# Performance work log

Hardware: AMD Instinct MI355X
Metric: run time of the kernel (lower is better)

The kernel has to match this reference:

```python
import math
import jax, jax.numpy as jnp
import numpy as np
from jax import lax

B, T, C = 2, 4096, 2048
N_HEAD, N_KV, D = 16, 4, 128
WINDOW, DILATION, CHUNK = 256, 1, 128


def make_rope_cache(seq_len, n_elem, base=10000.0):
    theta = 1.0 / base ** (jnp.arange(0, n_elem, 2, dtype=jnp.float32) / n_elem)
    idx_theta = jnp.arange(seq_len, dtype=jnp.float32)[:, None] * theta[None, :]
    return jnp.stack([jnp.cos(idx_theta), jnp.sin(idx_theta)], axis=-1)  # [T, n_elem/2, 2]


def setup_inputs() -> dict:
    key = jax.random.key(0)
    ks = jax.random.split(key, 5)
    s = 1.0 / math.sqrt(C)
    return {
        "x": jax.random.normal(ks[0], (B, T, C), dtype=jnp.float32),
        "wq": jax.random.normal(ks[1], (N_HEAD * D, C), dtype=jnp.float32) * s,
        "wk": jax.random.normal(ks[2], (N_KV * D, C), dtype=jnp.float32) * s,
        "wv": jax.random.normal(ks[3], (N_KV * D, C), dtype=jnp.float32) * s,
        "wo": jax.random.normal(ks[4], (N_HEAD * D, C), dtype=jnp.float32).T * s,  # stored [out,in]
        "rope_cache": make_rope_cache(T, D),
    }


def apply_rope(xh, cache):
    # xh: [B, T, H, D]; cache: [T, D/2, 2]
    b, t, h, d = xh.shape
    xr = xh.reshape(b, t, h, d // 2, 2)
    cos = cache[:t, :, 0][None, :, None, :]
    sin = cache[:t, :, 1][None, :, None, :]
    x0, x1 = xr[..., 0], xr[..., 1]
    rot = jnp.stack([x0 * cos - x1 * sin, x0 * sin + x1 * cos], axis=-1)
    return rot.reshape(b, t, h, d)


def sliding_attention(q, k, v, window, dilation, chunk):
    # q,k,v: [B, H, T, D] -> [B, H, T, D]; O(T*window), memory bounded via scan over chunks
    b, h, t, d = q.shape
    w = min(window, (t + dilation - 1) // dilation)
    offsets = jnp.arange(w) * dilation
    scale = 1.0 / math.sqrt(d)
    n_chunks = t // chunk

    def step(carry, c):
        pos = c * chunk + jnp.arange(chunk)                       # [L]
        idx_raw = (pos - (w - 1) * dilation)[:, None] + offsets[None, :]  # [L, w]
        invalid = idx_raw < 0
        idx = jnp.clip(idx_raw, 0, t - 1)
        flat = idx.reshape(-1)
        k_win = jnp.take(k, flat, axis=2).reshape(b, h, chunk, w, d)
        v_win = jnp.take(v, flat, axis=2).reshape(b, h, chunk, w, d)
        q_c = lax.dynamic_slice_in_dim(q, c * chunk, chunk, axis=2)
        scores = jnp.einsum('bhld,bhlwd->bhlw', q_c.astype(jnp.float32),
                            k_win.astype(jnp.float32)) * scale
        scores = jnp.where(invalid[None, None], -jnp.inf, scores)
        attn = jax.nn.softmax(scores, axis=-1)
        out_c = jnp.einsum('bhlw,bhlwd->bhld', attn, v_win.astype(jnp.float32))
        return carry, out_c.astype(q.dtype)

    _, outs = lax.scan(step, None, jnp.arange(n_chunks))  # [n_chunks, B, H, chunk, D]
    return outs.transpose(1, 2, 0, 3, 4).reshape(b, h, t, d)


def reference(x, wq, wk, wv, wo, rope_cache):
    b, t, c = x.shape
    q = (x @ wq.T).reshape(b, t, N_HEAD, D)
    k = (x @ wk.T).reshape(b, t, N_KV, D)
    v = (x @ wv.T).reshape(b, t, N_KV, D)
    q = apply_rope(q, rope_cache)
    k = apply_rope(k, rope_cache)
    q = q.transpose(0, 2, 1, 3)  # [B, H, T, D]
    k = k.transpose(0, 2, 1, 3)
    v = v.transpose(0, 2, 1, 3)
    g = N_HEAD // N_KV
    k = jnp.repeat(k, g, axis=1)
    v = jnp.repeat(v, g, axis=1)
    y = sliding_attention(q, k, v, WINDOW, DILATION, CHUNK)
    y = y.transpose(0, 2, 1, 3).reshape(b, t, c)
    return y @ wo.T
```

## Files before the change

### kernel.cpp

```cpp
#include <hip/hip_runtime.h>
#include <stdint.h>

typedef unsigned short u16;
typedef __attribute__((ext_vector_type(8))) short bf16x8;
typedef __attribute__((ext_vector_type(8))) unsigned short u16x8;
typedef __attribute__((ext_vector_type(4))) float f32x4;

#define B_  2
#define T_  4096
#define C_  2048
#define NH  16
#define NKV 4
#define HD  128

__device__ __forceinline__ u16 f2bf(float f) {
  union { float f; uint32_t u; } v; v.f = f;
  uint32_t u = v.u;
  u += 0x7fffu + ((u >> 16) & 1u);
  return (u16)(u >> 16);
}
__device__ __forceinline__ float bf2f(u16 h) {
  union { uint32_t u; float f; } v; v.u = ((uint32_t)h) << 16;
  return v.f;
}

__device__ __forceinline__ void gload_lds16(const u16* g, u16* l) {
  __builtin_amdgcn_global_load_lds(
      (const __attribute__((address_space(1))) void*)g,
      (__attribute__((address_space(3))) void*)l, 16, 0, 0);
}

__global__ void cvt_f32_bf16(const float* __restrict__ src, u16* __restrict__ dst, int n) {
  int i = (blockIdx.x * blockDim.x + threadIdx.x) * 4;
  if (i >= n) return;
  float4 v = *(const float4*)(src + i);
  ushort4 o;
  o.x = f2bf(v.x); o.y = f2bf(v.y); o.z = f2bf(v.z); o.w = f2bf(v.w);
  *(ushort4*)(dst + i) = o;
}

__global__ void rope_kernel(u16* __restrict__ qkv, const float* __restrict__ cache) {
  const int PH = (NH + NKV) * (HD / 2);
  long idx = (long)blockIdx.x * blockDim.x + threadIdx.x;
  if (idx >= (long)B_ * T_ * PH) return;
  int row = (int)(idx / PH);
  int rem = (int)(idx % PH);
  int hh = rem >> 6;
  int i  = rem & 63;
  int t  = row & (T_ - 1);
  float sc = (hh < NH) ? 0.1275174315f : 1.0f;
  float c = cache[t * 128 + 2 * i] * sc;
  float s = cache[t * 128 + 2 * i + 1] * sc;
  u16* p = qkv + (long)row * 3072 + hh * HD + 2 * i;
  float x0 = bf2f(p[0]), x1 = bf2f(p[1]);
  p[0] = f2bf(x0 * c - x1 * s);
  p[1] = f2bf(x0 * s + x1 * c);
}

__global__ void krearr(const u16* __restrict__ qkv, u16* __restrict__ K2) {
  int gid = blockIdx.x * 256 + threadIdx.x;
  int r = gid & 65535, bk = gid >> 16;
  int l16 = r & 15, q4 = (r >> 4) & 3, ks = (r >> 6) & 3, kb = r >> 8;
  int bb = bk >> 2, kv = bk & 3;
  const u16* src = qkv + ((long)(bb * T_ + kb * 16 + l16)) * 3072 + 2048 + kv * HD +
                   ks * 32 + q4 * 8;
  *(u16x8*)(K2 + (long)bk * 524288 + (long)r * 8) = *(const u16x8*)src;
}

__global__ void vrearr(const u16* __restrict__ qkv, u16* __restrict__ V2) {
  int gid = blockIdx.x * 256 + threadIdx.x;
  int r = gid & 65535, bk = gid >> 16;
  int l16 = r & 15, q4 = (r >> 4) & 3, ks = (r >> 6) & 3, jd = (r >> 8) & 7, kc = r >> 11;
  int bb = bk >> 2, kv = bk & 3;
  int key0 = kc * 128 + ks * 32 + q4 * 8;
  int d = jd * 16 + l16;
  const u16* src = qkv + ((long)(bb * T_ + key0)) * 3072 + 2560 + kv * HD + d;
  u16x8 v;
#pragma unroll
  for (int e = 0; e < 8; e++) v[e] = src[(long)e * 3072];
  *(u16x8*)(V2 + (long)bk * 524288 + (long)r * 8) = v;
}

#define GBAR() __builtin_amdgcn_s_barrier()
#define LGKM0() do { asm volatile("s_waitcnt lgkmcnt(0)" ::: "memory"); \
                     __builtin_amdgcn_sched_barrier(0); } while (0)

template <int WRITE_BF16>
__global__ __launch_bounds__(512, 2) void gemm256(const u16* __restrict__ A,
                                                  const u16* __restrict__ Bw,
                                                  void* __restrict__ Cv,
                                                  int M, int N, int K) {
  __shared__ u16 lds[65536];
  const int tid = threadIdx.x;
  const int lane = tid & 63;
  const int wave = tid >> 6;
  const int q4 = lane >> 4, l16 = lane & 15;
  const int wm = wave >> 2, wn = wave & 3;

  const int nwg = gridDim.x * gridDim.y;
  const int orig = blockIdx.y * gridDim.x + blockIdx.x;
  const int swz = (orig & 7) * (nwg >> 3) + (orig >> 3);
  const int bm = swz / gridDim.x, bn = swz % gridDim.x;
  const long m0 = (long)bm * 256, n0 = (long)bn * 256;

  const int srow = tid >> 2;
  const int slot = tid & 3;
  const int sx = (slot ^ ((srow >> 1) & 3)) * 8;
  const u16* Ag0 = A + (m0 + srow) * K + sx;
  const u16* Ag1 = A + (m0 + srow + 128) * K + sx;
  const u16* Bg0 = Bw + (n0 + srow) * K + sx;
  const u16* Bg1 = Bw + (n0 + srow + 128) * K + sx;
  u16* ldst = lds + tid * 8;

  const int nkt = K >> 6;

#define STAGE_A(bufi, kh, kt)                                  \
  do {                                                         \
    long ko = ((long)(kt) << 6) + ((kh) << 5);                 \
    u16* d = ldst + (bufi) * 32768 + (kh) * 8192;              \
    gload_lds16(Ag0 + ko, d);                                  \
    gload_lds16(Ag1 + ko, d + 4096);                           \
  } while (0)
#define STAGE_B(bufi, kh, kt)                                  \
  do {                                                         \
    long ko = ((long)(kt) << 6) + ((kh) << 5);                 \
    u16* d = ldst + (bufi) * 32768 + 16384 + (kh) * 8192;      \
    gload_lds16(Bg0 + ko, d);                                  \
    gload_lds16(Bg1 + ko, d + 4096);                           \
  } while (0)

  int offA[8], offB[4];
#pragma unroll
  for (int m = 0; m < 8; m++) {
    int r = wm * 128 + m * 16 + l16;
    offA[m] = r * 32 + ((q4 ^ ((r >> 1) & 3)) << 3);
  }
#pragma unroll
  for (int n = 0; n < 4; n++) {
    int r = wn * 64 + n * 16 + l16;
    offB[n] = 16384 + r * 32 + ((q4 ^ ((r >> 1) & 3)) << 3);
  }

  f32x4 acc[8][4] = {};

  STAGE_A(0, 0, 0); STAGE_B(0, 0, 0); STAGE_A(0, 1, 0); STAGE_B(0, 1, 0);
  if (nkt > 1) {
    STAGE_A(1, 0, 1); STAGE_B(1, 0, 1);
    asm volatile("s_waitcnt vmcnt(4)" ::: "memory");
  } else {
    asm volatile("s_waitcnt vmcnt(0)" ::: "memory");
  }
  GBAR();

  bf16x8 afX[4], afY[4], bvA[4], bvB[4];
  for (int kt = 0; kt < nkt; kt++) {
    const int bo = (kt & 1) * 32768;
#pragma unroll
    for (int m = 0; m < 4; m++) afX[m] = *(const bf16x8*)(lds + bo + offA[m]);
#pragma unroll
    for (int n = 0; n < 4; n++) bvA[n] = *(const bf16x8*)(lds + bo + offB[n]);
    if (kt + 1 < nkt) STAGE_A((kt + 1) & 1, 1, kt + 1);
    LGKM0();
#pragma unroll
    for (int m = 0; m < 4; m++) afY[m] = *(const bf16x8*)(lds + bo + offA[4 + m]);
    __builtin_amdgcn_s_setprio(1);
#pragma unroll
    for (int m = 0; m < 4; m++)
#pragma unroll
      for (int n = 0; n < 4; n++)
        acc[m][n] = __builtin_amdgcn_mfma_f32_16x16x32_bf16(afX[m], bvA[n], acc[m][n], 0, 0, 0);
    __builtin_amdgcn_s_setprio(0);
    if (kt + 1 < nkt) STAGE_B((kt + 1) & 1, 1, kt + 1);
    LGKM0();
#pragma unroll
    for (int m = 0; m < 4; m++) afX[m] = *(const bf16x8*)(lds + bo + 8192 + offA[m]);
#pragma unroll
    for (int n = 0; n < 4; n++) bvB[n] = *(const bf16x8*)(lds + bo + 8192 + offB[n]);
    __builtin_amdgcn_s_setprio(1);
#pragma unroll
    for (int m = 0; m < 4; m++)
#pragma unroll
      for (int n = 0; n < 4; n++)
        acc[4 + m][n] = __builtin_amdgcn_mfma_f32_16x16x32_bf16(afY[m], bvA[n], acc[4 + m][n], 0, 0, 0);
    __builtin_amdgcn_s_setprio(0);
    GBAR();
    if (kt + 2 < nkt) STAGE_A(kt & 1, 0, kt + 2);
    LGKM0();
#pragma unroll
    for (int m = 0; m < 4; m++) afY[m] = *(const bf16x8*)(lds + bo + 8192 + offA[4 + m]);
    __builtin_amdgcn_s_setprio(1);
#pragma unroll
    for (int m = 0; m < 4; m++)
#pragma unroll
      for (int n = 0; n < 4; n++)
        acc[m][n] = __builtin_amdgcn_mfma_f32_16x16x32_bf16(afX[m], bvB[n], acc[m][n], 0, 0, 0);
    __builtin_amdgcn_s_setprio(0);
    if (kt + 2 < nkt) STAGE_B(kt & 1, 0, kt + 2);
    LGKM0();
    __builtin_amdgcn_s_setprio(1);
#pragma unroll
    for (int m = 0; m < 4; m++)
#pragma unroll
      for (int n = 0; n < 4; n++)
        acc[4 + m][n] = __builtin_amdgcn_mfma_f32_16x16x32_bf16(afY[m], bvB[n], acc[4 + m][n], 0, 0, 0);
    __builtin_amdgcn_s_setprio(0);
    if (kt + 2 < nkt)
      asm volatile("s_waitcnt vmcnt(4)" ::: "memory");
    else
      asm volatile("s_waitcnt vmcnt(0)" ::: "memory");
    GBAR();
  }
#undef STAGE_A
#undef STAGE_B

  const long crow0 = m0 + wm * 128;
  const long ccol0 = n0 + wn * 64;
  if (WRITE_BF16) {
    u16* Cp = (u16*)Cv;
#pragma unroll
    for (int m = 0; m < 8; m++)
#pragma unroll
      for (int n = 0; n < 4; n++)
#pragma unroll
        for (int r = 0; r < 4; r++)
          Cp[(crow0 + m * 16 + q4 * 4 + r) * (long)N + ccol0 + n * 16 + l16] =
              f2bf(acc[m][n][r]);
  } else {
    float* Cp = (float*)Cv;
#pragma unroll
    for (int m = 0; m < 8; m++)
#pragma unroll
      for (int n = 0; n < 4; n++)
#pragma unroll
        for (int r = 0; r < 4; r++)
          Cp[(crow0 + m * 16 + q4 * 4 + r) * (long)N + ccol0 + n * 16 + l16] =
              acc[m][n][r];
  }
}

__global__ __launch_bounds__(256, 3) void attn_kernel(const u16* __restrict__ qkv,
                                                      const u16* __restrict__ K2,
                                                      const u16* __restrict__ V2,
                                                      u16* __restrict__ y) {
  const int tc = blockIdx.x, h = blockIdx.y, b = blockIdx.z;
  const int t0 = tc * 128;
  const int kvh = h >> 2;
  __shared__ u16 Pl[4 * 32 * 136];
  const int tid = threadIdx.x, wave = tid >> 6, lane = tid & 63;
  const int q4 = lane >> 4, l16 = lane & 15;
  u16* Pw = Pl + wave * (32 * 136);

  bf16x8 qf[2][4];
#pragma unroll
  for (int i = 0; i < 2; i++)
#pragma unroll
    for (int ks = 0; ks < 4; ks++)
      qf[i][ks] = *(const bf16x8*)(qkv +
          ((long)(b * T_ + t0 + 32 * wave + 16 * i + l16)) * 3072 + h * HD + ks * 32 + q4 * 8);

  f32x4 O[2][8] = {};
  float l_i[2][4] = {};

  const u16* Kb = K2 + (long)(b * NKV + kvh) * 524288 + lane * 8;
  const u16* Vb = V2 + (long)(b * NKV + kvh) * 524288 + lane * 8;

  int kstart = t0 - 256; if (kstart < 0) kstart = 0;
  for (int k0 = kstart; k0 <= t0; k0 += 128) {
    const u16* Kc = Kb + (long)(k0 >> 4) * 2048;
    const u16* Vc = Vb + (long)(k0 >> 7) * 16384;
    const int dbase0 = t0 + 32 * wave + q4 * 4 - k0 - l16;
    bf16x8 kn[4];
#pragma unroll
    for (int ks = 0; ks < 4; ks++) kn[ks] = *(const bf16x8*)(Kc + ks * 512);
#pragma unroll
    for (int j = 0; j < 8; j++) {
      bf16x8 kf[4];
#pragma unroll
      for (int ks = 0; ks < 4; ks++) kf[ks] = kn[ks];
      if (j < 7)
#pragma unroll
        for (int ks = 0; ks < 4; ks++)
          kn[ks] = *(const bf16x8*)(Kc + (j + 1) * 2048 + ks * 512);
      f32x4 s0 = {}, s1 = {};
#pragma unroll
      for (int ks = 0; ks < 4; ks++) {
        s0 = __builtin_amdgcn_mfma_f32_16x16x32_bf16(qf[0][ks], kf[ks], s0, 0, 0, 0);
        s1 = __builtin_amdgcn_mfma_f32_16x16x32_bf16(qf[1][ks], kf[ks], s1, 0, 0, 0);
      }
#pragma unroll
      for (int r = 0; r < 4; r++) {
        int d0 = dbase0 + r - 16 * j;
        float p0 = __builtin_amdgcn_exp2f(s0[r]);
        p0 = ((unsigned)d0 <= 255u) ? p0 : 0.f;
        l_i[0][r] += p0;
        Pw[(q4 * 4 + r) * 136 + 16 * j + l16] = f2bf(p0);
        int d1 = d0 + 16;
        float p1 = __builtin_amdgcn_exp2f(s1[r]);
        p1 = ((unsigned)d1 <= 255u) ? p1 : 0.f;
        l_i[1][r] += p1;
        Pw[(16 + q4 * 4 + r) * 136 + 16 * j + l16] = f2bf(p1);
      }
    }
    bf16x8 vn = *(const bf16x8*)(Vc);
#pragma unroll
    for (int ks = 0; ks < 4; ks++) {
      bf16x8 pf0 = *(const bf16x8*)(&Pw[l16 * 136 + ks * 32 + q4 * 8]);
      bf16x8 pf1 = *(const bf16x8*)(&Pw[(16 + l16) * 136 + ks * 32 + q4 * 8]);
#pragma unroll
      for (int jd = 0; jd < 8; jd++) {
        bf16x8 vf = vn;
        if (!(ks == 3 && jd == 7)) {
          int njd = (jd == 7) ? 0 : jd + 1;
          int nks = (jd == 7) ? ks + 1 : ks;
          vn = *(const bf16x8*)(Vc + (njd * 4 + nks) * 512);
        }
        O[0][jd] = __builtin_amdgcn_mfma_f32_16x16x32_bf16(pf0, vf, O[0][jd], 0, 0, 0);
        O[1][jd] = __builtin_amdgcn_mfma_f32_16x16x32_bf16(pf1, vf, O[1][jd], 0, 0, 0);
      }
    }
  }
#pragma unroll
  for (int d = 1; d < 16; d <<= 1)
#pragma unroll
    for (int i = 0; i < 2; i++)
#pragma unroll
      for (int r = 0; r < 4; r++)
        l_i[i][r] += __shfl_xor(l_i[i][r], d, 64);
#pragma unroll
  for (int i = 0; i < 2; i++)
#pragma unroll
    for (int r = 0; r < 4; r++) {
      float inv = 1.0f / l_i[i][r];
      long row = (long)(b * T_ + t0 + 32 * wave + 16 * i + q4 * 4 + r);
#pragma unroll
      for (int jd = 0; jd < 8; jd++)
        y[row * 2048 + h * HD + 16 * jd + l16] = f2bf(O[i][jd][r] * inv);
    }
}

extern "C" void kernel_launch(void* const* d_in, const int* in_sizes, int n_in,
                              void* d_out, int out_size, void* d_ws, size_t ws_size,
                              hipStream_t stream) {
  const float* x    = (const float*)d_in[0];
  const float* wq   = (const float*)d_in[1];
  const float* wk   = (const float*)d_in[2];
  const float* wv   = (const float*)d_in[3];
  const float* wo   = (const float*)d_in[4];
  const float* rope = (const float*)d_in[5];
  float* out = (float*)d_out;

  u16* xb   = (u16*)d_ws;
  u16* wqkv = xb + (long)8192 * 2048;
  u16* wob  = wqkv + (long)3072 * 2048;
  u16* qkv  = wob + (long)2048 * 2048;
  u16* V2   = qkv + (long)8192 * 3072;
  u16* K2   = wqkv;
  u16* yb   = xb;

  {
    long n = (long)8192 * 2048;
    cvt_f32_bf16<<<dim3((unsigned)((n / 4 + 255) / 256)), dim3(256), 0, stream>>>(x, xb, (int)n);
    n = (long)2048 * 2048;
    cvt_f32_bf16<<<dim3((unsigned)((n / 4 + 255) / 256)), dim3(256), 0, stream>>>(wq, wqkv, (int)n);
    n = (long)512 * 2048;
    cvt_f32_bf16<<<dim3((unsigned)((n / 4 + 255) / 256)), dim3(256), 0, stream>>>(
        wk, wqkv + (long)2048 * 2048, (int)n);
    cvt_f32_bf16<<<dim3((unsigned)((n / 4 + 255) / 256)), dim3(256), 0, stream>>>(
        wv, wqkv + (long)2048 * 2048 + (long)512 * 2048, (int)n);
    n = (long)2048 * 2048;
    cvt_f32_bf16<<<dim3((unsigned)((n / 4 + 255) / 256)), dim3(256), 0, stream>>>(wo, wob, (int)n);
  }

  gemm256<1><<<dim3(3072 / 256, 8192 / 256), dim3(512), 0, stream>>>(
      xb, wqkv, (void*)qkv, 8192, 3072, 2048);

  long npairs = (long)B_ * T_ * (NH + NKV) * (HD / 2);
  rope_kernel<<<dim3((unsigned)((npairs + 255) / 256)), dim3(256), 0, stream>>>(qkv, rope);

  krearr<<<dim3(2048), dim3(256), 0, stream>>>(qkv, K2);
  vrearr<<<dim3(2048), dim3(256), 0, stream>>>(qkv, V2);

  attn_kernel<<<dim3(T_ / 128, NH, B_), dim3(256), 0, stream>>>(qkv, K2, V2, yb);

  gemm256<0><<<dim3(2048 / 256, 8192 / 256), dim3(512), 0, stream>>>(
      yb, wob, (void*)out, 8192, 2048, 2048);
}
```

Before: 446.7 us.

## Fuse RoPE into QKV GEMM epilogue and switch to 128x256 tiles

Removes the standalone RoPE kernel and applies the rotation and the Q scale in the QKV GEMM epilogue, using lane shuffles to pair adjacent columns. This saves one read-modify-write pass over the Q/K activations. The GEMM is also restructured from 512-thread 256x256 tiles with a two-deep K pipeline to 256-thread 128x256 tiles with a K step of 32 and a full vmcnt(0) wait every iteration. That change reduces latency hiding and per-block reuse in exchange for smaller LDS use and more blocks.

```diff
diff --git a/kernel.cpp b/kernel.cpp
--- a/kernel.cpp
+++ b/kernel.cpp
@@ -37,24 +37,6 @@
   ushort4 o;
   o.x = f2bf(v.x); o.y = f2bf(v.y); o.z = f2bf(v.z); o.w = f2bf(v.w);
   *(ushort4*)(dst + i) = o;
-}
-
-__global__ void rope_kernel(u16* __restrict__ qkv, const float* __restrict__ cache) {
-  const int PH = (NH + NKV) * (HD / 2);
-  long idx = (long)blockIdx.x * blockDim.x + threadIdx.x;
-  if (idx >= (long)B_ * T_ * PH) return;
-  int row = (int)(idx / PH);
-  int rem = (int)(idx % PH);
-  int hh = rem >> 6;
-  int i  = rem & 63;
-  int t  = row & (T_ - 1);
-  float sc = (hh < NH) ? 0.1275174315f : 1.0f;
-  float c = cache[t * 128 + 2 * i] * sc;
-  float s = cache[t * 128 + 2 * i + 1] * sc;
-  u16* p = qkv + (long)row * 3072 + hh * HD + 2 * i;
-  float x0 = bf2f(p[0]), x1 = bf2f(p[1]);
-  p[0] = f2bf(x0 * c - x1 * s);
-  p[1] = f2bf(x0 * s + x1 * c);
 }
 
 __global__ void krearr(const u16* __restrict__ qkv, u16* __restrict__ K2) {
@@ -85,81 +67,86 @@
 #define LGKM0() do { asm volatile("s_waitcnt lgkmcnt(0)" ::: "memory"); \
                      __builtin_amdgcn_sched_barrier(0); } while (0)
 
-template <int WRITE_BF16>
-__global__ __launch_bounds__(512, 2) void gemm256(const u16* __restrict__ A,
+template <int WRITE_BF16, int ROPE>
+__global__ __launch_bounds__(256, 2) void gemm128(const u16* __restrict__ A,
                                                   const u16* __restrict__ Bw,
                                                   void* __restrict__ Cv,
+                                                  const float* __restrict__ rope,
                                                   int M, int N, int K) {
-  __shared__ u16 lds[65536];
+  __shared__ u16 lds[24576];
   const int tid = threadIdx.x;
   const int lane = tid & 63;
   const int wave = tid >> 6;
   const int q4 = lane >> 4, l16 = lane & 15;
-  const int wm = wave >> 2, wn = wave & 3;
 
   const int nwg = gridDim.x * gridDim.y;
   const int orig = blockIdx.y * gridDim.x + blockIdx.x;
   const int swz = (orig & 7) * (nwg >> 3) + (orig >> 3);
   const int bm = swz / gridDim.x, bn = swz % gridDim.x;
-  const long m0 = (long)bm * 256, n0 = (long)bn * 256;
+  const long m0 = (long)bm * 128, n0 = (long)bn * 256;
 
   const int srow = tid >> 2;
   const int slot = tid & 3;
-  const int sx = (slot ^ ((srow >> 1) & 3)) * 8;
-  const u16* Ag0 = A + (m0 + srow) * K + sx;
-  const u16* Ag1 = A + (m0 + srow + 128) * K + sx;
-  const u16* Bg0 = Bw + (n0 + srow) * K + sx;
-  const u16* Bg1 = Bw + (n0 + srow + 128) * K + sx;
+  const int sx = (slot ^ ((srow >> 1) & 3)) << 3;
+  const u16* Ag0 = A + (m0 + srow) * (long)K + sx;
+  const u16* Ag1 = A + (m0 + 64 + srow) * (long)K + sx;
+  const u16* Bg0 = Bw + (n0 + srow) * (long)K + sx;
+  const u16* Bg1 = Bw + (n0 + 64 + srow) * (long)K + sx;
+  const u16* Bg2 = Bw + (n0 + 128 + srow) * (long)K + sx;
+  const u16* Bg3 = Bw + (n0 + 192 + srow) * (long)K + sx;
   u16* ldst = lds + tid * 8;
 
-  const int nkt = K >> 6;
-
-#define STAGE_A(bufi, kh, kt)                                  \
-  do {                                                         \
-    long ko = ((long)(kt) << 6) + ((kh) << 5);                 \
-    u16* d = ldst + (bufi) * 32768 + (kh) * 8192;              \
-    gload_lds16(Ag0 + ko, d);                                  \
-    gload_lds16(Ag1 + ko, d + 4096);                           \
+  const int nkt = K >> 5;
+
+#define STAGE_A(bufi, kt)                                       \
+  do {                                                          \
+    long ko = (long)(kt) << 5;                                  \
+    u16* d = ldst + (bufi) * 12288;                             \
+    gload_lds16(Ag0 + ko, d);                                   \
+    gload_lds16(Ag1 + ko, d + 2048);                            \
   } while (0)
-#define STAGE_B(bufi, kh, kt)                                  \
-  do {                                                         \
-    long ko = ((long)(kt) << 6) + ((kh) << 5);                 \
-    u16* d = ldst + (bufi) * 32768 + 16384 + (kh) * 8192;      \
-    gload_lds16(Bg0 + ko, d);                                  \
-    gload_lds16(Bg1 + ko, d + 4096);                           \
+#define STAGE_B01(bufi, kt)                                     \
+  do {                                                          \
+    long ko = (long)(kt) << 5;                                  \
+    u16* d = ldst + (bufi) * 12288 + 4096;                      \
+    gload_lds16(Bg0 + ko, d);                                   \
+    gload_lds16(Bg1 + ko, d + 2048);                            \
   } while (0)
+#define STAGE_B23(bufi, kt)                                     \
+  do {                                                          \
+    long ko = (long)(kt) << 5;                                  \
+    u16* d = ldst + (bufi) * 12288 + 4096;                      \
+    gload_lds16(Bg2 + ko, d + 4096);                            \
+    gload_lds16(Bg3 + ko, d + 6144);                            \
+  } while (0)
 
   int offA[8], offB[4];
 #pragma unroll
   for (int m = 0; m < 8; m++) {
-    int r = wm * 128 + m * 16 + l16;
+    int r = m * 16 + l16;
     offA[m] = r * 32 + ((q4 ^ ((r >> 1) & 3)) << 3);
   }
 #pragma unroll
   for (int n = 0; n < 4; n++) {
-    int r = wn * 64 + n * 16 + l16;
-    offB[n] = 16384 + r * 32 + ((q4 ^ ((r >> 1) & 3)) << 3);
+    int r = wave * 64 + n * 16 + l16;
+    offB[n] = 4096 + r * 32 + ((q4 ^ ((r >> 1) & 3)) << 3);
   }
 
   f32x4 acc[8][4] = {};
 
-  STAGE_A(0, 0, 0); STAGE_B(0, 0, 0); STAGE_A(0, 1, 0); STAGE_B(0, 1, 0);
-  if (nkt > 1) {
-    STAGE_A(1, 0, 1); STAGE_B(1, 0, 1);
-    asm volatile("s_waitcnt vmcnt(4)" ::: "memory");
-  } else {
-    asm volatile("s_waitcnt vmcnt(0)" ::: "memory");
-  }
+  STAGE_A(0, 0); STAGE_B01(0, 0); STAGE_B23(0, 0);
+  asm volatile("s_waitcnt vmcnt(0)" ::: "memory");
   GBAR();
 
-  bf16x8 afX[4], afY[4], bvA[4], bvB[4];
+  bf16x8 afX[4], afY[4], bv[4];
   for (int kt = 0; kt < nkt; kt++) {
-    const int bo = (kt & 1) * 32768;
+    const int bo = (kt & 1) * 12288;
+    const int nx = (kt & 1) ^ 1;
 #pragma unroll
     for (int m = 0; m < 4; m++) afX[m] = *(const bf16x8*)(lds + bo + offA[m]);
 #pragma unroll
-    for (int n = 0; n < 4; n++) bvA[n] = *(const bf16x8*)(lds + bo + offB[n]);
-    if (kt + 1 < nkt) STAGE_A((kt + 1) & 1, 1, kt + 1);
+    for (int n = 0; n < 4; n++) bv[n] = *(const bf16x8*)(lds + bo + offB[n]);
+    if (kt + 1 < nkt) { STAGE_A(nx, kt + 1); STAGE_B01(nx, kt + 1); }
     LGKM0();
 #pragma unroll
     for (int m = 0; m < 4; m++) afY[m] = *(const bf16x8*)(lds + bo + offA[4 + m]);
@@ -168,74 +155,50 @@
     for (int m = 0; m < 4; m++)
 #pragma unroll
       for (int n = 0; n < 4; n++)
-        acc[m][n] = __builtin_amdgcn_mfma_f32_16x16x32_bf16(afX[m], bvA[n], acc[m][n], 0, 0, 0);
+        acc[m][n] = __builtin_amdgcn_mfma_f32_16x16x32_bf16(afX[m], bv[n], acc[m][n], 0, 0, 0);
     __builtin_amdgcn_s_setprio(0);
-    if (kt + 1 < nkt) STAGE_B((kt + 1) & 1, 1, kt + 1);
-    LGKM0();
-#pragma unroll
-    for (int m = 0; m < 4; m++) afX[m] = *(const bf16x8*)(lds + bo + 8192 + offA[m]);
-#pragma unroll
-    for (int n = 0; n < 4; n++) bvB[n] = *(const bf16x8*)(lds + bo + 8192 + offB[n]);
-    __builtin_amdgcn_s_setprio(1);
-#pragma unroll
-    for (int m = 0; m < 4; m++)
-#pragma unroll
-      for (int n = 0; n < 4; n++)
-        acc[4 + m][n] = __builtin_amdgcn_mfma_f32_16x16x32_bf16(afY[m], bvA[n], acc[4 + m][n], 0, 0, 0);
-    __builtin_amdgcn_s_setprio(0);
-    GBAR();
-    if (kt + 2 < nkt) STAGE_A(kt & 1, 0, kt + 2);
-    LGKM0();
-#pragma unroll
-    for (int m = 0; m < 4; m++) afY[m] = *(const bf16x8*)(lds + bo + 8192 + offA[4 + m]);
-    __builtin_amdgcn_s_setprio(1);
-#pragma unroll
-    for (int m = 0; m < 4; m++)
-#pragma unroll
-      for (int n = 0; n < 4; n++)
-        acc[m][n] = __builtin_amdgcn_mfma_f32_16x16x32_bf16(afX[m], bvB[n], acc[m][n], 0, 0, 0);
-    __builtin_amdgcn_s_setprio(0);
-    if (kt + 2 < nkt) STAGE_B(kt & 1, 0, kt + 2);
+    if (kt + 1 < nkt) STAGE_B23(nx, kt + 1);
     LGKM0();
     __builtin_amdgcn_s_setprio(1);
 #pragma unroll
     for (int m = 0; m < 4; m++)
 #pragma unroll
       for (int n = 0; n < 4; n++)
-        acc[4 + m][n] = __builtin_amdgcn_mfma_f32_16x16x32_bf16(afY[m], bvB[n], acc[4 + m][n], 0, 0, 0);
+        acc[4 + m][n] = __builtin_amdgcn_mfma_f32_16x16x32_bf16(afY[m], bv[n], acc[4 + m][n], 0, 0, 0);
     __builtin_amdgcn_s_setprio(0);
-    if (kt + 2 < nkt)
-      asm volatile("s_waitcnt vmcnt(4)" ::: "memory");
-    else
-      asm volatile("s_waitcnt vmcnt(0)" ::: "memory");
+    asm volatile("s_waitcnt vmcnt(0)" ::: "memory");
     GBAR();
   }
 #undef STAGE_A
-#undef STAGE_B
-
-  const long crow0 = m0 + wm * 128;
-  const long ccol0 = n0 + wn * 64;
-  if (WRITE_BF16) {
-    u16* Cp = (u16*)Cv;
-#pragma unroll
-    for (int m = 0; m < 8; m++)
-#pragma unroll
-      for (int n = 0; n < 4; n++)
-#pragma unroll
-        for (int r = 0; r < 4; r++)
-          Cp[(crow0 + m * 16 + q4 * 4 + r) * (long)N + ccol0 + n * 16 + l16] =
-              f2bf(acc[m][n][r]);
-  } else {
-    float* Cp = (float*)Cv;
-#pragma unroll
-    for (int m = 0; m < 8; m++)
-#pragma unroll
-      for (int n = 0; n < 4; n++)
-#pragma unroll
-        for (int r = 0; r < 4; r++)
-          Cp[(crow0 + m * 16 + q4 * 4 + r) * (long)N + ccol0 + n * 16 + l16] =
-              acc[m][n][r];
-  }
+#undef STAGE_B01
+#undef STAGE_B23
+
+  const long ccol0 = n0 + wave * 64;
+#pragma unroll
+  for (int m = 0; m < 8; m++)
+#pragma unroll
+    for (int n = 0; n < 4; n++) {
+      const int cfrag = (int)(ccol0 + n * 16);
+#pragma unroll
+      for (int r = 0; r < 4; r++) {
+        long row = m0 + m * 16 + q4 * 4 + r;
+        float x = acc[m][n][r];
+        if (ROPE && cfrag < 2560) {
+          int tt = (int)row & (T_ - 1);
+          int c = cfrag + l16;
+          float cv = rope[tt * 128 + (c & 127)];
+          float px = __shfl_xor(x, 1, 64);
+          float pcv = __shfl_xor(cv, 1, 64);
+          float rot = ((l16 & 1) == 0) ? (x * cv - px * pcv) : (px * cv + x * pcv);
+          if (cfrag < 2048) rot *= 0.1275174315f;
+          x = rot;
+        }
+        if (WRITE_BF16)
+          ((u16*)Cv)[row * (long)N + ccol0 + n * 16 + l16] = f2bf(x);
+        else
+          ((float*)Cv)[row * (long)N + ccol0 + n * 16 + l16] = x;
+      }
+    }
 }
 
 __global__ __launch_bounds__(256, 3) void attn_kernel(const u16* __restrict__ qkv,
@@ -371,17 +334,14 @@
     cvt_f32_bf16<<<dim3((unsigned)((n / 4 + 255) / 256)), dim3(256), 0, stream>>>(wo, wob, (int)n);
   }
 
-  gemm256<1><<<dim3(3072 / 256, 8192 / 256), dim3(512), 0, stream>>>(
-      xb, wqkv, (void*)qkv, 8192, 3072, 2048);
-
-  long npairs = (long)B_ * T_ * (NH + NKV) * (HD / 2);
-  rope_kernel<<<dim3((unsigned)((npairs + 255) / 256)), dim3(256), 0, stream>>>(qkv, rope);
+  gemm128<1, 1><<<dim3(3072 / 256, 8192 / 128), dim3(256), 0, stream>>>(
+      xb, wqkv, (void*)qkv, rope, 8192, 3072, 2048);
 
   krearr<<<dim3(2048), dim3(256), 0, stream>>>(qkv, K2);
   vrearr<<<dim3(2048), dim3(256), 0, stream>>>(qkv, V2);
 
   attn_kernel<<<dim3(T_ / 128, NH, B_), dim3(256), 0, stream>>>(qkv, K2, V2, yb);
 
-  gemm256<0><<<dim3(2048 / 256, 8192 / 256), dim3(512), 0, stream>>>(
-      yb, wob, (void*)out, 8192, 2048, 2048);
-}
+  gemm128<0, 0><<<dim3(2048 / 256, 8192 / 128), dim3(256), 0, stream>>>(
+      yb, wob, (void*)out, (const float*)nullptr, 8192, 2048, 2048);
+}
```

Result: slower. 506.5 us (+13.4%).

## Fuse RoPE into QKV GEMM epilogue, merge casts, LDS-staged V rearrange

Applied to the files above, without the earlier changes.

Merges the five fp32-to-bf16 conversion launches into a single kernel and folds the RoPE rotation and query scaling into the QKV GEMM epilogue, using lane shuffles to pair elements. This removes one full read-modify-write pass over the QKV buffer. The V rearrangement now stages a 128-key tile in LDS so global reads are coalesced, replacing the strided per-element gathers. The epilogue gains extra cache loads and shuffles, which may add register pressure to the GEMM.

```diff
diff --git a/kernel.cpp b/kernel.cpp
--- a/kernel.cpp
+++ b/kernel.cpp
@@ -30,31 +30,21 @@
       (__attribute__((address_space(3))) void*)l, 16, 0, 0);
 }
 
-__global__ void cvt_f32_bf16(const float* __restrict__ src, u16* __restrict__ dst, int n) {
-  int i = (blockIdx.x * blockDim.x + threadIdx.x) * 4;
-  if (i >= n) return;
-  float4 v = *(const float4*)(src + i);
-  ushort4 o;
-  o.x = f2bf(v.x); o.y = f2bf(v.y); o.z = f2bf(v.z); o.w = f2bf(v.w);
-  *(ushort4*)(dst + i) = o;
-}
-
-__global__ void rope_kernel(u16* __restrict__ qkv, const float* __restrict__ cache) {
-  const int PH = (NH + NKV) * (HD / 2);
-  long idx = (long)blockIdx.x * blockDim.x + threadIdx.x;
-  if (idx >= (long)B_ * T_ * PH) return;
-  int row = (int)(idx / PH);
-  int rem = (int)(idx % PH);
-  int hh = rem >> 6;
-  int i  = rem & 63;
-  int t  = row & (T_ - 1);
-  float sc = (hh < NH) ? 0.1275174315f : 1.0f;
-  float c = cache[t * 128 + 2 * i] * sc;
-  float s = cache[t * 128 + 2 * i + 1] * sc;
-  u16* p = qkv + (long)row * 3072 + hh * HD + 2 * i;
-  float x0 = bf2f(p[0]), x1 = bf2f(p[1]);
-  p[0] = f2bf(x0 * c - x1 * s);
-  p[1] = f2bf(x0 * s + x1 * c);
+__global__ void cvt_all(const float* __restrict__ x, const float* __restrict__ wq,
+                        const float* __restrict__ wk, const float* __restrict__ wv,
+                        const float* __restrict__ wo, u16* __restrict__ xb,
+                        u16* __restrict__ wqkv, u16* __restrict__ wob) {
+  long i = ((long)blockIdx.x * 256 + threadIdx.x) * 4;
+  const float* src; u16* dst; long off;
+  if (i < 16777216L)      { src = x;  dst = xb;              off = i; }
+  else if (i < 20971520L) { src = wq; dst = wqkv;            off = i - 16777216L; }
+  else if (i < 22020096L) { src = wk; dst = wqkv + 4194304L; off = i - 20971520L; }
+  else if (i < 23068672L) { src = wv; dst = wqkv + 5242880L; off = i - 22020096L; }
+  else                    { src = wo; dst = wob;             off = i - 23068672L; }
+  float4 v = *(const float4*)(src + off);
+  ushort4 o4;
+  o4.x = f2bf(v.x); o4.y = f2bf(v.y); o4.z = f2bf(v.z); o4.w = f2bf(v.w);
+  *(ushort4*)(dst + off) = o4;
 }
 
 __global__ void krearr(const u16* __restrict__ qkv, u16* __restrict__ K2) {
@@ -67,28 +57,46 @@
   *(u16x8*)(K2 + (long)bk * 524288 + (long)r * 8) = *(const u16x8*)src;
 }
 
-__global__ void vrearr(const u16* __restrict__ qkv, u16* __restrict__ V2) {
-  int gid = blockIdx.x * 256 + threadIdx.x;
-  int r = gid & 65535, bk = gid >> 16;
-  int l16 = r & 15, q4 = (r >> 4) & 3, ks = (r >> 6) & 3, jd = (r >> 8) & 7, kc = r >> 11;
-  int bb = bk >> 2, kv = bk & 3;
-  int key0 = kc * 128 + ks * 32 + q4 * 8;
-  int d = jd * 16 + l16;
-  const u16* src = qkv + ((long)(bb * T_ + key0)) * 3072 + 2560 + kv * HD + d;
-  u16x8 v;
-#pragma unroll
-  for (int e = 0; e < 8; e++) v[e] = src[(long)e * 3072];
-  *(u16x8*)(V2 + (long)bk * 524288 + (long)r * 8) = v;
+__global__ __launch_bounds__(256) void vrearr2(const u16* __restrict__ qkv,
+                                               u16* __restrict__ V2) {
+  const int bid = blockIdx.x;
+  const int bk = bid >> 5, kc = bid & 31;
+  const int bb = bk >> 2, kv = bk & 3;
+  const int t = threadIdx.x;
+  __shared__ u16 L[128 * 136];
+  {
+    int key = t >> 1;
+    int dh = (t & 1) * 64;
+    const u16* src = qkv + ((long)(bb * T_ + kc * 128 + key)) * 3072 + 2560 + kv * HD + dh;
+    u16* dst = L + key * 136 + dh;
+#pragma unroll
+    for (int u = 0; u < 8; u++)
+      *(u16x8*)(dst + u * 8) = *(const u16x8*)(src + u * 8);
+  }
+  __syncthreads();
+  u16* out = V2 + (long)bk * 524288 + (long)kc * 16384;
+#pragma unroll
+  for (int step = 0; step < 8; step++) {
+    int o = step * 256 + t;
+    int l16 = o & 15, q4 = (o >> 4) & 3, ks = (o >> 6) & 3, jd = (o >> 8) & 7;
+    int keyb = ks * 32 + q4 * 8;
+    int d = jd * 16 + l16;
+    u16x8 v;
+#pragma unroll
+    for (int e = 0; e < 8; e++) v[e] = L[(keyb + e) * 136 + d];
+    *(u16x8*)(out + (long)o * 8) = v;
+  }
 }
 
 #define GBAR() __builtin_amdgcn_s_barrier()
 #define LGKM0() do { asm volatile("s_waitcnt lgkmcnt(0)" ::: "memory"); \
                      __builtin_amdgcn_sched_barrier(0); } while (0)
 
-template <int WRITE_BF16>
+template <int WRITE_BF16, int ROPE>
 __global__ __launch_bounds__(512, 2) void gemm256(const u16* __restrict__ A,
                                                   const u16* __restrict__ Bw,
                                                   void* __restrict__ Cv,
+                                                  const float* __restrict__ rope,
                                                   int M, int N, int K) {
   __shared__ u16 lds[65536];
   const int tid = threadIdx.x;
@@ -215,27 +223,31 @@
 
   const long crow0 = m0 + wm * 128;
   const long ccol0 = n0 + wn * 64;
-  if (WRITE_BF16) {
-    u16* Cp = (u16*)Cv;
-#pragma unroll
-    for (int m = 0; m < 8; m++)
-#pragma unroll
-      for (int n = 0; n < 4; n++)
-#pragma unroll
-        for (int r = 0; r < 4; r++)
-          Cp[(crow0 + m * 16 + q4 * 4 + r) * (long)N + ccol0 + n * 16 + l16] =
-              f2bf(acc[m][n][r]);
-  } else {
-    float* Cp = (float*)Cv;
-#pragma unroll
-    for (int m = 0; m < 8; m++)
-#pragma unroll
-      for (int n = 0; n < 4; n++)
-#pragma unroll
-        for (int r = 0; r < 4; r++)
-          Cp[(crow0 + m * 16 + q4 * 4 + r) * (long)N + ccol0 + n * 16 + l16] =
-              acc[m][n][r];
-  }
+#pragma unroll
+  for (int m = 0; m < 8; m++)
+#pragma unroll
+    for (int n = 0; n < 4; n++) {
+      const int cfrag = (int)(ccol0 + n * 16);
+#pragma unroll
+      for (int r = 0; r < 4; r++) {
+        long row = crow0 + m * 16 + q4 * 4 + r;
+        float x = acc[m][n][r];
+        if (ROPE && cfrag < 2560) {
+          int tt = (int)row & (T_ - 1);
+          int c = cfrag + l16;
+          float cv = rope[tt * 128 + (c & 127)];
+          float px = __shfl_xor(x, 1, 64);
+          float pcv = __shfl_xor(cv, 1, 64);
+          float rot = ((l16 & 1) == 0) ? (x * cv - px * pcv) : (px * cv + x * pcv);
+          if (cfrag < 2048) rot *= 0.1275174315f;
+          x = rot;
+        }
+        if (WRITE_BF16)
+          ((u16*)Cv)[row * (long)N + ccol0 + n * 16 + l16] = f2bf(x);
+        else
+          ((float*)Cv)[row * (long)N + ccol0 + n * 16 + l16] = x;
+      }
+    }
 }
 
 __global__ __launch_bounds__(256, 3) void attn_kernel(const u16* __restrict__ qkv,
@@ -357,31 +369,16 @@
   u16* K2   = wqkv;
   u16* yb   = xb;
 
-  {
-    long n = (long)8192 * 2048;
-    cvt_f32_bf16<<<dim3((unsigned)((n / 4 + 255) / 256)), dim3(256), 0, stream>>>(x, xb, (int)n);
-    n = (long)2048 * 2048;
-    cvt_f32_bf16<<<dim3((unsigned)((n / 4 + 255) / 256)), dim3(256), 0, stream>>>(wq, wqkv, (int)n);
-    n = (long)512 * 2048;
-    cvt_f32_bf16<<<dim3((unsigned)((n / 4 + 255) / 256)), dim3(256), 0, stream>>>(
-        wk, wqkv + (long)2048 * 2048, (int)n);
-    cvt_f32_bf16<<<dim3((unsigned)((n / 4 + 255) / 256)), dim3(256), 0, stream>>>(
-        wv, wqkv + (long)2048 * 2048 + (long)512 * 2048, (int)n);
-    n = (long)2048 * 2048;
-    cvt_f32_bf16<<<dim3((unsigned)((n / 4 + 255) / 256)), dim3(256), 0, stream>>>(wo, wob, (int)n);
-  }
-
-  gemm256<1><<<dim3(3072 / 256, 8192 / 256), dim3(512), 0, stream>>>(
-      xb, wqkv, (void*)qkv, 8192, 3072, 2048);
-
-  long npairs = (long)B_ * T_ * (NH + NKV) * (HD / 2);
-  rope_kernel<<<dim3((unsigned)((npairs + 255) / 256)), dim3(256), 0, stream>>>(qkv, rope);
+  cvt_all<<<dim3(26624), dim3(256), 0, stream>>>(x, wq, wk, wv, wo, xb, wqkv, wob);
+
+  gemm256<1, 1><<<dim3(3072 / 256, 8192 / 256), dim3(512), 0, stream>>>(
+      xb, wqkv, (void*)qkv, rope, 8192, 3072, 2048);
 
   krearr<<<dim3(2048), dim3(256), 0, stream>>>(qkv, K2);
-  vrearr<<<dim3(2048), dim3(256), 0, stream>>>(qkv, V2);
+  vrearr2<<<dim3(256), dim3(256), 0, stream>>>(qkv, V2);
 
   attn_kernel<<<dim3(T_ / 128, NH, B_), dim3(256), 0, stream>>>(qkv, K2, V2, yb);
 
-  gemm256<0><<<dim3(2048 / 256, 8192 / 256), dim3(512), 0, stream>>>(
-      yb, wob, (void*)out, 8192, 2048, 2048);
-}
+  gemm256<0, 0><<<dim3(2048 / 256, 8192 / 256), dim3(512), 0, stream>>>(
+      yb, wob, (void*)out, (const float*)nullptr, 8192, 2048, 2048);
+}
```

Measured after the change: 501.2 us. 1.12x slower.
